# Kernel optimization log

Measured on AMD Instinct MI355X. Metric: run time of the kernel, lower is better.

Reference implementation:

```python
import jax, jax.numpy as jnp
import numpy as np

B, N, K, M, CIN, O, OUT = 4, 1024, 30, 8, 9, 64, 512
BN_SCALE = 1.0 / np.sqrt(1.0 + 1e-5)  # eval-mode BatchNorm with default stats/affine


def setup_inputs() -> dict:
    key = jax.random.key(0)
    ks = jax.random.split(key, 8)
    x = jax.random.normal(ks[0], (B, CIN, N), jnp.float32)
    norm_plt = jax.random.normal(ks[1], (B, 3, N), jnp.float32)
    cls_label = jnp.zeros((B, 16), jnp.float32)
    conv1_w = jax.random.normal(ks[2], (64, 18), jnp.float32) * np.sqrt(2.0 / 18.0)
    conv1_b = jnp.zeros((64,), jnp.float32)
    sn_hw = jax.random.normal(ks[3], (4, 16, 28), jnp.float32) * np.sqrt(2.0 / 28.0)
    sn_ow = jax.random.normal(ks[4], (4, M, 16), jnp.float32) * np.sqrt(2.0 / 16.0)
    sn_ob = jnp.zeros((4, M), jnp.float32)
    mats = jax.random.normal(ks[5], (4, 2 * O, M * O), jnp.float32) * np.sqrt(2.0 / (2.0 * O))
    convt_w = jax.random.normal(ks[6], (OUT, 5 * O), jnp.float32) * np.sqrt(2.0 / (5.0 * O))
    return dict(x=x, norm_plt=norm_plt, cls_label=cls_label, conv1_w=conv1_w,
                conv1_b=conv1_b, sn_hw=sn_hw, sn_ow=sn_ow, sn_ob=sn_ob,
                mats=mats, convt_w=convt_w)


def _gather(feat, idx):
    # feat (B,N,C), idx (B,N,K) int -> (B,N,K,C): neighbor feature gather
    return jax.vmap(lambda f, i: f[i])(feat, idx)


def _bn(t):
    return t * BN_SCALE


def reference(x, norm_plt, cls_label, conv1_w, conv1_b, sn_hw, sn_ow, sn_ob, mats, convt_w):
    xt = jnp.transpose(x, (0, 2, 1))                       # (B,N,9)
    sq = jnp.sum(xt * xt, axis=-1)
    neg_d = 2.0 * jnp.einsum('bic,bjc->bij', xt, xt) - sq[:, :, None] - sq[:, None, :]
    _, idx = jax.lax.top_k(neg_d, K)                       # (B,N,K) knn indices

    nbr = _gather(xt, idx)                                 # (B,N,K,9)
    ctr = jnp.broadcast_to(xt[:, :, None, :], nbr.shape)   # (B,N,K,9)
    diff = nbr - ctr
    ed = jnp.linalg.norm(diff, axis=-1, keepdims=True)     # (B,N,K,1)
    xyz = jnp.concatenate([diff, nbr, ctr, ed], axis=-1)   # (B,N,K,28) scorenet input

    # get_graph_feature -> conv1 (1x1) -> BN -> relu -> max over k
    gf = jnp.concatenate([diff, ctr], axis=-1)             # (B,N,K,18)
    h = jax.nn.relu(_bn(jnp.einsum('bnkc,oc->bnko', gf, conv1_w) + conv1_b))
    x1 = jnp.max(h, axis=2)                                # (B,N,64)

    feats = [x1]
    f = x1
    for l in range(4):  # PAConv layers 2..5 (sequential, fixed count)
        hid = jax.nn.relu(_bn(jnp.einsum('bnkc,hc->bnkh', xyz, sn_hw[l])))
        score = jax.nn.softmax(jnp.einsum('bnkh,mh->bnkm', hid, sn_ow[l]) + sn_ob[l], axis=-1)
        kern = mats[l]                                     # (128, M*64)
        # feat_trans_dgcnn: neighbor uses full kernel on [f;f], center uses top half
        point = (jnp.concatenate([f, f], axis=-1) @ kern).reshape(B, N, M, O)
        center = (f @ kern[:O]).reshape(B, N, M, O)
        # assemble_dgcnn: sum_k sum_m score * (point[knn] - center)
        gp = _gather(point.reshape(B, N, M * O), idx).reshape(B, N, K, M, O)
        out = jnp.einsum('bnkm,bnkmo->bno', score, gp) - jnp.einsum('bnkm,bnmo->bno', score, center)
        f = jax.nn.relu(_bn(out))
        feats.append(f)

    xx = jnp.concatenate(feats, axis=-1)                   # (B,N,320)
    xc = jax.nn.relu(_bn(jnp.einsum('bnc,oc->bno', xx, convt_w)))
    return jnp.max(xc, axis=1)                             # (B,512) global max pool
```

## Files before the change

### kernel.cpp

```cpp
#include <hip/hip_runtime.h>
#include <hip/hip_bf16.h>

#define B 4
#define N 1024
#define KNN 30
#define MM 8
#define HID 16
#define FD 320
#define OUTC 512
#define BNS 0.9999950000374997f

typedef float f32x4 __attribute__((ext_vector_type(4)));
typedef short s16x8 __attribute__((ext_vector_type(8)));

#define OFF_XT16 0
#define OFF_XTT  65536
#define OFF_SQ   102400
#define OFF_IDX  106496
#define OFF_CVT  229376
#define OFF_K2T  311296
#define OFF_FB   442368
#define OFF_SC   1097728

__global__ void __launch_bounds__(256) k_prep(const float* __restrict__ x,
                                              const float* __restrict__ convt_w,
                                              const float* __restrict__ mats,
                                              float* __restrict__ xt16,
                                              float* __restrict__ xtT,
                                              float* __restrict__ sq,
                                              __hip_bfloat16* __restrict__ cvt_bf,
                                              __hip_bfloat16* __restrict__ k2t_bf,
                                              float* __restrict__ out) {
  __shared__ float tile[64][65];
  if (blockIdx.x < 640) {
    int id = blockIdx.x * 256 + threadIdx.x;
    if (id < B * N) {
      int b = id >> 10, n = id & 1023;
      float s = 0.f;
#pragma unroll
      for (int c = 0; c < 9; c++) {
        float v = x[(b * 9 + c) * N + n];
        xt16[id * 16 + c] = v;
        xtT[c * 4096 + id] = v;
        s = fmaf(v, v, s);
      }
      sq[id] = s;
    }
    if (id < B * OUTC) out[id] = 0.f;
    if (id < 512 * 320) cvt_bf[id] = __float2bfloat16(convt_w[id]);
  } else {
    int blk = blockIdx.x - 640;
    int l = blk >> 4, part = (blk >> 3) & 1, m = blk & 7;
    int tr = threadIdx.x >> 6, tc = threadIdx.x & 63;
    const float* src = mats + l * 65536 + (part * 64) * 512 + m * 64;
#pragma unroll
    for (int it = 0; it < 16; it++) { int c = it * 4 + tr; tile[c][tc] = src[c * 512 + tc]; }
    __syncthreads();
    __hip_bfloat16* dst = k2t_bf + l * 65536 + part * 512 + m * 64;
#pragma unroll
    for (int it = 0; it < 16; it++) { int o = it * 4 + tr; dst[o * 1024 + tc] = __float2bfloat16(tile[tc][o]); }
  }
}

__global__ void __launch_bounds__(256) k_knnc1(const float* __restrict__ xt16,
                                               const float* __restrict__ xtT,
                                               const float* __restrict__ sq,
                                               const float* __restrict__ w,
                                               const float* __restrict__ bias,
                                               int* __restrict__ idx,
                                               __hip_bfloat16* __restrict__ feats_bf) {
  int t = threadIdx.x;
  int r = t >> 6;
  int lane = t & 63;
  int row = blockIdx.x * 4 + r;
  int b = row >> 10;
  __shared__ unsigned int hist[4][256];
  __shared__ unsigned int bp[4];
  __shared__ int bn[4];
  __shared__ int js_l[4][KNN];
  __shared__ float ws[64 * 18];
  __shared__ __align__(16) float diff_s[4][KNN][12];
  __shared__ float ctr_s[4][9];
  for (int i = t; i < 64 * 18; i += 256) ws[i] = w[i];
  if (t < 36) { int rr = t / 9, c = t - rr * 9; ctr_s[rr][c] = xt16[(blockIdx.x * 4 + rr) * 16 + c]; }
  const float* xtb = xtT + (b << 10);
  float cx[9];
#pragma unroll
  for (int c = 0; c < 9; c++) cx[c] = xt16[row * 16 + c];
  float sqn = sq[row];
  unsigned int key[16];
#pragma unroll
  for (int s = 0; s < 16; s++) {
    int j = s * 64 + lane;
    float dot = 0.f;
#pragma unroll
    for (int c = 0; c < 9; c++) dot = fmaf(cx[c], xtb[c * 4096 + j], dot);
    float v = 2.0f * dot - sqn - sq[(b << 10) + j];
    unsigned u = __float_as_uint(v);
    key[s] = u ^ ((unsigned)(((int)u) >> 31) | 0x80000000u);
  }
  unsigned prefix = 0; int need = KNN;
  for (int p = 0; p < 4; p++) {
    int shift = 24 - 8 * p;
    for (int i = lane; i < 256; i += 64) hist[r][i] = 0;
    __syncthreads();
    unsigned himask = p ? (0xFFFFFFFFu << (shift + 8)) : 0u;
#pragma unroll
    for (int s = 0; s < 16; s++)
      if ((key[s] & himask) == prefix) atomicAdd(&hist[r][(key[s] >> shift) & 255], 1u);
    __syncthreads();
    int c0 = hist[r][4 * lane], c1 = hist[r][4 * lane + 1];
    int c2 = hist[r][4 * lane + 2], c3 = hist[r][4 * lane + 3];
    int lsum = c0 + c1 + c2 + c3, sfx = lsum;
#pragma unroll
    for (int ofs = 1; ofs < 64; ofs <<= 1) {
      int tt = __shfl_down(sfx, ofs, 64);
      if (lane + ofs < 64) sfx += tt;
    }
    int A3 = sfx - lsum, A2 = A3 + c3, A1 = A2 + c2, A0 = A1 + c1;
    if (A0 < need && need <= A0 + c0) { bp[r] = prefix | ((unsigned)(4 * lane + 0) << shift); bn[r] = need - A0; }
    if (A1 < need && need <= A1 + c1) { bp[r] = prefix | ((unsigned)(4 * lane + 1) << shift); bn[r] = need - A1; }
    if (A2 < need && need <= A2 + c2) { bp[r] = prefix | ((unsigned)(4 * lane + 2) << shift); bn[r] = need - A2; }
    if (A3 < need && need <= A3 + c3) { bp[r] = prefix | ((unsigned)(4 * lane + 3) << shift); bn[r] = need - A3; }
    __syncthreads();
    prefix = bp[r]; need = bn[r];
  }
  unsigned T = prefix;
  int* orow = idx + row * KNN;
  unsigned long long lowmask = (1ull << lane) - 1ull;
  int aboveBase = 0;
#pragma unroll
  for (int s = 0; s < 16; s++) {
    unsigned long long mA = __ballot(key[s] > T);
    if (key[s] > T) {
      int slot = aboveBase + __popcll(mA & lowmask);
      orow[slot] = s * 64 + lane;
      js_l[r][slot] = s * 64 + lane;
    }
    aboveBase += __popcll(mA);
  }
  int tieBase = 0;
  for (int s = 0; s < 16 && tieBase < need; s++) {
    unsigned long long mT = __ballot(key[s] == T);
    if (key[s] == T) {
      int rk = tieBase + __popcll(mT & lowmask);
      if (rk < need) {
        orow[aboveBase + rk] = s * 64 + lane;
        js_l[r][aboveBase + rk] = s * 64 + lane;
      }
    }
    tieBase += __popcll(mT);
  }
  __syncthreads();
  if (t < 120) {
    int rr = t / KNN, k = t - rr * KNN;
    int jg = (b << 10) + js_l[rr][k];
#pragma unroll
    for (int c = 0; c < 9; c++) diff_s[rr][k][c] = xt16[jg * 16 + c] - ctr_s[rr][c];
  }
  __syncthreads();
  float wd[9];
#pragma unroll
  for (int c = 0; c < 9; c++) wd[c] = ws[lane * 18 + c];
  float cd = 0.f;
#pragma unroll
  for (int c = 0; c < 9; c++) cd = fmaf(ctr_s[r][c], ws[lane * 18 + 9 + c], cd);
  float best = -3.0e38f;
  for (int k = 0; k < KNN; k++) {
    const f32x4* dr = (const f32x4*)diff_s[r][k];
    f32x4 d0 = dr[0], d1 = dr[1], d2 = dr[2];
    float dd = 0.f;
    dd = fmaf(d0.x, wd[0], dd); dd = fmaf(d0.y, wd[1], dd);
    dd = fmaf(d0.z, wd[2], dd); dd = fmaf(d0.w, wd[3], dd);
    dd = fmaf(d1.x, wd[4], dd); dd = fmaf(d1.y, wd[5], dd);
    dd = fmaf(d1.z, wd[6], dd); dd = fmaf(d1.w, wd[7], dd);
    dd = fmaf(d2.x, wd[8], dd);
    best = fmaxf(best, dd);
  }
  float val = (best + cd + bias[lane]) * BNS;
  feats_bf[row * FD + lane] = __float2bfloat16(fmaxf(val, 0.f));
}

__global__ void __launch_bounds__(256) k_score(const float* __restrict__ xt16,
                                               const int* __restrict__ idx,
                                               const float* __restrict__ hw,
                                               const float* __restrict__ ow,
                                               const float* __restrict__ ob,
                                               float* __restrict__ score) {
  __shared__ float hws[4 * 448];
  __shared__ float ows[4 * 128];
  __shared__ float obs[32];
  int t = threadIdx.x;
  for (int i = t; i < 1792; i += 256) hws[i] = hw[i];
  for (int i = t; i < 512; i += 256) ows[i] = ow[i];
  if (t < 32) obs[t] = ob[t];
  __syncthreads();
  int id = blockIdx.x * 256 + t;
  int row = id / KNN;
  int b = row >> 10;
  int jg = (b << 10) + idx[id];
  const float* xc = xt16 + row * 16;
  const float* xj = xt16 + jg * 16;
  float xv[28];
  float d2 = 0.f;
#pragma unroll
  for (int c = 0; c < 9; c++) {
    float nb = xj[c], ct = xc[c], df = nb - ct;
    xv[c] = df; xv[9 + c] = nb; xv[18 + c] = ct;
    d2 = fmaf(df, df, d2);
  }
  xv[27] = sqrtf(d2);
  for (int l = 0; l < 4; l++) {
    float hid[HID];
#pragma unroll
    for (int h = 0; h < HID; h++) {
      float a = 0.f;
#pragma unroll
      for (int c = 0; c < 28; c++) a = fmaf(xv[c], hws[l * 448 + h * 28 + c], a);
      hid[h] = fmaxf(a * BNS, 0.f);
    }
    float lg[MM], mx = -3.0e38f;
#pragma unroll
    for (int m = 0; m < MM; m++) {
      float a = obs[l * 8 + m];
#pragma unroll
      for (int h = 0; h < HID; h++) a = fmaf(hid[h], ows[l * 128 + m * 16 + h], a);
      lg[m] = a; mx = fmaxf(mx, a);
    }
    float s = 0.f;
#pragma unroll
    for (int m = 0; m < MM; m++) { lg[m] = __expf(lg[m] - mx); s += lg[m]; }
    float inv = 1.0f / s;
    float* so = score + l * 983040 + id * 8;
    *(float4*)so = make_float4(lg[0] * inv, lg[1] * inv, lg[2] * inv, lg[3] * inv);
    *(float4*)(so + 4) = make_float4(lg[4] * inv, lg[5] * inv, lg[6] * inv, lg[7] * inv);
  }
}

#define HSTR 1048
__global__ void __launch_bounds__(512) k_layer2(const int* __restrict__ idx,
                                                const float* __restrict__ score,
                                                const __hip_bfloat16* __restrict__ k2t_bf,
                                                __hip_bfloat16* __restrict__ feats_bf,
                                                const __hip_bfloat16* __restrict__ cvt_bf,
                                                float* __restrict__ out,
                                                int l, int last) {
  int row0 = blockIdx.x * 16;
  int t = threadIdx.x;
  int b = row0 >> 10;
  __shared__ int js[16][KNN];
  __shared__ float ssum[16][8];
  __shared__ __align__(16) __hip_bfloat16 Hs[16][HSTR];
  __shared__ __align__(16) __hip_bfloat16 ftile[16][336];
  __shared__ float pacc[8][16][16];
  const float* sc_l = score + l * 983040;
  for (int i = t; i < 16 * KNN; i += 512) {
    int r = i / KNN, k = i - r * KNN;
    js[r][k] = (b << 10) + idx[(row0 + r) * KNN + k];
  }
  if (t < 128) {
    int r = t >> 3, m = t & 7;
    float a = 0.f;
    for (int k = 0; k < KNN; k++) a += sc_l[(row0 + r) * 240 + k * 8 + m];
    ssum[r][m] = a;
  }
  __syncthreads();
  int w = t >> 6, lane = t & 63;
#pragma unroll
  for (int rr = 0; rr < 2; rr++) {
    int r = w * 2 + rr;
    int row = row0 + r;
    const float4* srow = (const float4*)(sc_l + row * 240);
    float g[MM] = {};
#pragma unroll
    for (int k = 0; k < KNN; k++) {
      float fv = __bfloat162float(feats_bf[js[r][k] * FD + l * 64 + lane]);
      float4 s0 = srow[2 * k], s1 = srow[2 * k + 1];
      g[0] = fmaf(s0.x, fv, g[0]); g[1] = fmaf(s0.y, fv, g[1]);
      g[2] = fmaf(s0.z, fv, g[2]); g[3] = fmaf(s0.w, fv, g[3]);
      g[4] = fmaf(s1.x, fv, g[4]); g[5] = fmaf(s1.y, fv, g[5]);
      g[6] = fmaf(s1.z, fv, g[6]); g[7] = fmaf(s1.w, fv, g[7]);
    }
    float fn = __bfloat162float(feats_bf[row * FD + l * 64 + lane]);
#pragma unroll
    for (int m = 0; m < MM; m++) {
      Hs[r][m * 64 + lane] = __float2bfloat16(g[m] - ssum[r][m] * fn);
      Hs[r][512 + m * 64 + lane] = __float2bfloat16(g[m]);
    }
  }
  if (last) {
    const short* Fs = (const short*)feats_bf;
    for (int i = t; i < 512; i += 512) {}
    for (int i = t; i < 512; i += 512) {}
    for (int i = t; i < 512; i += 512) {}
  }
  __syncthreads();
  if (last) {
    const short* Fs = (const short*)feats_bf;
    for (int i = t; i < 512; i += 512) {
      int r = i >> 5, c8 = (i & 31) * 8;
      *(s16x8*)&ftile[r][c8] = *(const s16x8*)(Fs + (row0 + r) * FD + c8);
    }
    __syncthreads();
  }
  int lr = lane & 15, lk8 = (lane >> 4) * 8;
  {
    int ct = w & 3, kh = w >> 2;
    const short* Ks2 = (const short*)(k2t_bf + l * 65536);
    const short* brow = Ks2 + (ct * 16 + lr) * 1024 + kh * 512 + lk8;
    const short* arow = (const short*)&Hs[lr][kh * 512 + lk8];
    f32x4 acc = {0.f, 0.f, 0.f, 0.f};
#pragma unroll 8
    for (int kk = 0; kk < 16; kk++) {
      s16x8 a = *(const s16x8*)(arow + kk * 32);
      s16x8 bb = *(const s16x8*)(brow + kk * 32);
      acc = __builtin_amdgcn_mfma_f32_16x16x32_bf16(a, bb, acc, 0, 0, 0);
    }
#pragma unroll
    for (int i = 0; i < 4; i++)
      pacc[w][(lane >> 4) * 4 + i][lr] = acc[i];
  }
  __syncthreads();
  if (w < 4) {
#pragma unroll
    for (int i = 0; i < 4; i++) {
      int ri = (lane >> 4) * 4 + i;
      float val = fmaxf((pacc[w][ri][lr] + pacc[w + 4][ri][lr]) * BNS, 0.f);
      __hip_bfloat16 vb = __float2bfloat16(val);
      if (!last) {
        feats_bf[(row0 + ri) * FD + (l + 1) * 64 + w * 16 + lr] = vb;
      } else {
        ftile[ri][256 + w * 16 + lr] = vb;
      }
    }
  }
  if (last) {
    __syncthreads();
    const short* Ws = (const short*)cvt_bf;
#pragma unroll
    for (int tn = 0; tn < 4; tn++) {
      int nb = w * 64 + tn * 16;
      const short* brow = Ws + (nb + lr) * FD + lk8;
      const short* arow = (const short*)&ftile[lr][lk8];
      f32x4 acc = {0.f, 0.f, 0.f, 0.f};
#pragma unroll
      for (int kk = 0; kk < 10; kk++) {
        s16x8 a = *(const s16x8*)(arow + kk * 32);
        s16x8 bb = *(const s16x8*)(brow + kk * 32);
        acc = __builtin_amdgcn_mfma_f32_16x16x32_bf16(a, bb, acc, 0, 0, 0);
      }
      float mx = fmaxf(fmaxf(acc[0], acc[1]), fmaxf(acc[2], acc[3]));
      mx = fmaxf(mx, __shfl_xor(mx, 16, 64));
      mx = fmaxf(mx, __shfl_xor(mx, 32, 64));
      if ((lane >> 4) == 0) {
        float val = fmaxf(mx * BNS, 0.f);
        atomicMax((unsigned int*)out + b * OUTC + nb + lr, __float_as_uint(val));
      }
    }
  }
}

extern "C" void kernel_launch(void* const* d_in, const int* in_sizes, int n_in,
                              void* d_out, int out_size, void* d_ws, size_t ws_size,
                              hipStream_t stream) {
  const float* x       = (const float*)d_in[0];
  const float* conv1_w = (const float*)d_in[3];
  const float* conv1_b = (const float*)d_in[4];
  const float* sn_hw   = (const float*)d_in[5];
  const float* sn_ow   = (const float*)d_in[6];
  const float* sn_ob   = (const float*)d_in[7];
  const float* mats    = (const float*)d_in[8];
  const float* convt_w = (const float*)d_in[9];
  float* out = (float*)d_out;

  float* wsp = (float*)d_ws;
  float* xt16 = wsp + OFF_XT16;
  float* xtT  = wsp + OFF_XTT;
  float* sq   = wsp + OFF_SQ;
  int* idx    = (int*)(wsp + OFF_IDX);
  __hip_bfloat16* cvt_bf = (__hip_bfloat16*)(wsp + OFF_CVT);
  __hip_bfloat16* k2t_bf = (__hip_bfloat16*)(wsp + OFF_K2T);
  __hip_bfloat16* feats_bf = (__hip_bfloat16*)(wsp + OFF_FB);
  float* score = wsp + OFF_SC;

  k_prep<<<704, 256, 0, stream>>>(x, convt_w, mats, xt16, xtT, sq, cvt_bf, k2t_bf, out);
  k_knnc1<<<1024, 256, 0, stream>>>(xt16, xtT, sq, conv1_w, conv1_b, idx, feats_bf);
  k_score<<<480, 256, 0, stream>>>(xt16, idx, sn_hw, sn_ow, sn_ob, score);
  for (int l = 0; l < 4; l++) {
    k_layer2<<<256, 512, 0, stream>>>(idx, score, k2t_bf, feats_bf, cvt_bf, out,
                                      l, l == 3 ? 1 : 0);
  }
}
```

Measured before the change: 192.9 us.

## Fuse kNN, conv1 and ScoreNet into one kernel; precompute score sums

Removes the transposed x buffers: the kNN kernel now reads x directly and computes squared norms inline. ScoreNet softmax is folded into the same kernel, reusing the neighbor and diff values already staged in shared memory. The per-row score sums are computed there and passed to the layer kernels through a global buffer. This drops one launch and the intermediate traffic, but only 120 of 256 threads do the ScoreNet work, which may lengthen that kernel's critical path.

```diff
diff --git a/kernel.cpp b/kernel.cpp
--- a/kernel.cpp
+++ b/kernel.cpp
@@ -13,89 +13,94 @@
 typedef float f32x4 __attribute__((ext_vector_type(4)));
 typedef short s16x8 __attribute__((ext_vector_type(8)));
 
-#define OFF_XT16 0
-#define OFF_XTT  65536
-#define OFF_SQ   102400
-#define OFF_IDX  106496
-#define OFF_CVT  229376
-#define OFF_K2T  311296
-#define OFF_FB   442368
-#define OFF_SC   1097728
-
-__global__ void __launch_bounds__(256) k_prep(const float* __restrict__ x,
-                                              const float* __restrict__ convt_w,
-                                              const float* __restrict__ mats,
-                                              float* __restrict__ xt16,
-                                              float* __restrict__ xtT,
-                                              float* __restrict__ sq,
-                                              __hip_bfloat16* __restrict__ cvt_bf,
-                                              __hip_bfloat16* __restrict__ k2t_bf,
-                                              float* __restrict__ out) {
+#define OFF_IDX  0
+#define OFF_CVT  122880
+#define OFF_K2T  204800
+#define OFF_FB   335872
+#define OFF_SC   991232
+#define OFF_SSUM 4923392
+
+__global__ void __launch_bounds__(256) k_prep2(const float* __restrict__ mats,
+                                               const float* __restrict__ convt_w,
+                                               __hip_bfloat16* __restrict__ k2t_bf,
+                                               __hip_bfloat16* __restrict__ cvt_bf,
+                                               float* __restrict__ out) {
   __shared__ float tile[64][65];
-  if (blockIdx.x < 640) {
-    int id = blockIdx.x * 256 + threadIdx.x;
-    if (id < B * N) {
-      int b = id >> 10, n = id & 1023;
-      float s = 0.f;
-#pragma unroll
-      for (int c = 0; c < 9; c++) {
-        float v = x[(b * 9 + c) * N + n];
-        xt16[id * 16 + c] = v;
-        xtT[c * 4096 + id] = v;
-        s = fmaf(v, v, s);
-      }
-      sq[id] = s;
+  int t = threadIdx.x;
+  if (blockIdx.x < 64) {
+    int blk = blockIdx.x;
+    int l = blk >> 4, part = (blk >> 3) & 1, m = blk & 7;
+    int tr = t >> 6, tc = t & 63;
+    const float* src = mats + l * 65536 + (part * 64) * 512 + m * 64;
+#pragma unroll
+    for (int it = 0; it < 16; it++) { int c = it * 4 + tr; tile[c][tc] = src[c * 512 + tc]; }
+    __syncthreads();
+    __hip_bfloat16* dst = k2t_bf + l * 65536 + part * 512 + m * 64;
+#pragma unroll
+    for (int it = 0; it < 16; it++) { int o = it * 4 + tr; dst[o * 1024 + tc] = __float2bfloat16(tile[tc][o]); }
+  } else {
+    int id = (blockIdx.x - 64) * 256 + t;
+#pragma unroll
+    for (int q = 0; q < 4; q++) {
+      int i = id + q * 40960;
+      cvt_bf[i] = __float2bfloat16(convt_w[i]);
     }
     if (id < B * OUTC) out[id] = 0.f;
-    if (id < 512 * 320) cvt_bf[id] = __float2bfloat16(convt_w[id]);
-  } else {
-    int blk = blockIdx.x - 640;
-    int l = blk >> 4, part = (blk >> 3) & 1, m = blk & 7;
-    int tr = threadIdx.x >> 6, tc = threadIdx.x & 63;
-    const float* src = mats + l * 65536 + (part * 64) * 512 + m * 64;
-#pragma unroll
-    for (int it = 0; it < 16; it++) { int c = it * 4 + tr; tile[c][tc] = src[c * 512 + tc]; }
-    __syncthreads();
-    __hip_bfloat16* dst = k2t_bf + l * 65536 + part * 512 + m * 64;
-#pragma unroll
-    for (int it = 0; it < 16; it++) { int o = it * 4 + tr; dst[o * 1024 + tc] = __float2bfloat16(tile[tc][o]); }
   }
 }
 
-__global__ void __launch_bounds__(256) k_knnc1(const float* __restrict__ xt16,
-                                               const float* __restrict__ xtT,
-                                               const float* __restrict__ sq,
-                                               const float* __restrict__ w,
-                                               const float* __restrict__ bias,
-                                               int* __restrict__ idx,
-                                               __hip_bfloat16* __restrict__ feats_bf) {
+__global__ void __launch_bounds__(256) k1(const float* __restrict__ x,
+                                          const float* __restrict__ conv1_w,
+                                          const float* __restrict__ conv1_b,
+                                          const float* __restrict__ hw,
+                                          const float* __restrict__ ow,
+                                          const float* __restrict__ ob,
+                                          int* __restrict__ idx,
+                                          __hip_bfloat16* __restrict__ feats_bf,
+                                          float* __restrict__ score,
+                                          float* __restrict__ ssum_g) {
   int t = threadIdx.x;
-  int r = t >> 6;
-  int lane = t & 63;
+  int r = t >> 6, lane = t & 63;
   int row = blockIdx.x * 4 + r;
   int b = row >> 10;
   __shared__ unsigned int hist[4][256];
   __shared__ unsigned int bp[4];
   __shared__ int bn[4];
   __shared__ int js_l[4][KNN];
-  __shared__ float ws[64 * 18];
+  __shared__ float ws[1152];
+  __shared__ float hws[1792], ows[512], obs[32];
   __shared__ __align__(16) float diff_s[4][KNN][12];
+  __shared__ __align__(16) float nbr_s[4][KNN][12];
   __shared__ float ctr_s[4][9];
-  for (int i = t; i < 64 * 18; i += 256) ws[i] = w[i];
-  if (t < 36) { int rr = t / 9, c = t - rr * 9; ctr_s[rr][c] = xt16[(blockIdx.x * 4 + rr) * 16 + c]; }
-  const float* xtb = xtT + (b << 10);
+  __shared__ float scl[4][KNN][8];
+  const float* xb = x + b * 9216;
+
+  for (int i = t; i < 1152; i += 256) ws[i] = conv1_w[i];
+  for (int i = t; i < 1792; i += 256) hws[i] = hw[i];
+  if (t < 512) { }
+  for (int i = t; i < 512; i += 256) ows[i] = ow[i];
+  if (t < 32) obs[t] = ob[t];
+  if (t < 36) { int rr = t / 9, c = t - rr * 9; ctr_s[rr][c] = xb[c * 1024 + ((blockIdx.x * 4 + rr) & 1023)]; }
+
+  int jrow = row & 1023;
   float cx[9];
 #pragma unroll
-  for (int c = 0; c < 9; c++) cx[c] = xt16[row * 16 + c];
-  float sqn = sq[row];
+  for (int c = 0; c < 9; c++) cx[c] = xb[c * 1024 + jrow];
+  float sqn = 0.f;
+#pragma unroll
+  for (int c = 0; c < 9; c++) sqn = fmaf(cx[c], cx[c], sqn);
   unsigned int key[16];
 #pragma unroll
   for (int s = 0; s < 16; s++) {
     int j = s * 64 + lane;
-    float dot = 0.f;
-#pragma unroll
-    for (int c = 0; c < 9; c++) dot = fmaf(cx[c], xtb[c * 4096 + j], dot);
-    float v = 2.0f * dot - sqn - sq[(b << 10) + j];
+    float dot = 0.f, sbj = 0.f;
+#pragma unroll
+    for (int c = 0; c < 9; c++) {
+      float xjc = xb[c * 1024 + j];
+      dot = fmaf(cx[c], xjc, dot);
+      sbj = fmaf(xjc, xjc, sbj);
+    }
+    float v = 2.0f * dot - sqn - sbj;
     unsigned u = __float_as_uint(v);
     key[s] = u ^ ((unsigned)(((int)u) >> 31) | 0x80000000u);
   }
@@ -152,94 +157,102 @@
     tieBase += __popcll(mT);
   }
   __syncthreads();
+
   if (t < 120) {
     int rr = t / KNN, k = t - rr * KNN;
-    int jg = (b << 10) + js_l[rr][k];
-#pragma unroll
-    for (int c = 0; c < 9; c++) diff_s[rr][k][c] = xt16[jg * 16 + c] - ctr_s[rr][c];
-  }
-  __syncthreads();
-  float wd[9];
-#pragma unroll
-  for (int c = 0; c < 9; c++) wd[c] = ws[lane * 18 + c];
-  float cd = 0.f;
-#pragma unroll
-  for (int c = 0; c < 9; c++) cd = fmaf(ctr_s[r][c], ws[lane * 18 + 9 + c], cd);
-  float best = -3.0e38f;
-  for (int k = 0; k < KNN; k++) {
-    const f32x4* dr = (const f32x4*)diff_s[r][k];
-    f32x4 d0 = dr[0], d1 = dr[1], d2 = dr[2];
-    float dd = 0.f;
-    dd = fmaf(d0.x, wd[0], dd); dd = fmaf(d0.y, wd[1], dd);
-    dd = fmaf(d0.z, wd[2], dd); dd = fmaf(d0.w, wd[3], dd);
-    dd = fmaf(d1.x, wd[4], dd); dd = fmaf(d1.y, wd[5], dd);
-    dd = fmaf(d1.z, wd[6], dd); dd = fmaf(d1.w, wd[7], dd);
-    dd = fmaf(d2.x, wd[8], dd);
-    best = fmaxf(best, dd);
-  }
-  float val = (best + cd + bias[lane]) * BNS;
-  feats_bf[row * FD + lane] = __float2bfloat16(fmaxf(val, 0.f));
-}
-
-__global__ void __launch_bounds__(256) k_score(const float* __restrict__ xt16,
-                                               const int* __restrict__ idx,
-                                               const float* __restrict__ hw,
-                                               const float* __restrict__ ow,
-                                               const float* __restrict__ ob,
-                                               float* __restrict__ score) {
-  __shared__ float hws[4 * 448];
-  __shared__ float ows[4 * 128];
-  __shared__ float obs[32];
-  int t = threadIdx.x;
-  for (int i = t; i < 1792; i += 256) hws[i] = hw[i];
-  for (int i = t; i < 512; i += 256) ows[i] = ow[i];
-  if (t < 32) obs[t] = ob[t];
-  __syncthreads();
-  int id = blockIdx.x * 256 + t;
-  int row = id / KNN;
-  int b = row >> 10;
-  int jg = (b << 10) + idx[id];
-  const float* xc = xt16 + row * 16;
-  const float* xj = xt16 + jg * 16;
+    int j = js_l[rr][k];
+#pragma unroll
+    for (int c = 0; c < 9; c++) {
+      float nb = xb[c * 1024 + j];
+      nbr_s[rr][k][c] = nb;
+      diff_s[rr][k][c] = nb - ctr_s[rr][c];
+    }
+  }
+  __syncthreads();
+
+  {
+    float wd[9];
+#pragma unroll
+    for (int c = 0; c < 9; c++) wd[c] = ws[lane * 18 + c];
+    float cd = 0.f;
+#pragma unroll
+    for (int c = 0; c < 9; c++) cd = fmaf(ctr_s[r][c], ws[lane * 18 + 9 + c], cd);
+    float best = -3.0e38f;
+    for (int k = 0; k < KNN; k++) {
+      const f32x4* dr = (const f32x4*)diff_s[r][k];
+      f32x4 d0 = dr[0], d1 = dr[1], d2 = dr[2];
+      float dd = 0.f;
+      dd = fmaf(d0.x, wd[0], dd); dd = fmaf(d0.y, wd[1], dd);
+      dd = fmaf(d0.z, wd[2], dd); dd = fmaf(d0.w, wd[3], dd);
+      dd = fmaf(d1.x, wd[4], dd); dd = fmaf(d1.y, wd[5], dd);
+      dd = fmaf(d1.z, wd[6], dd); dd = fmaf(d1.w, wd[7], dd);
+      dd = fmaf(d2.x, wd[8], dd);
+      best = fmaxf(best, dd);
+    }
+    float val = (best + cd + conv1_b[lane]) * BNS;
+    feats_bf[row * FD + lane] = __float2bfloat16(fmaxf(val, 0.f));
+  }
+
   float xv[28];
-  float d2 = 0.f;
-#pragma unroll
-  for (int c = 0; c < 9; c++) {
-    float nb = xj[c], ct = xc[c], df = nb - ct;
-    xv[c] = df; xv[9 + c] = nb; xv[18 + c] = ct;
-    d2 = fmaf(df, df, d2);
-  }
-  xv[27] = sqrtf(d2);
+  int rrS = 0, kS = 0;
+  if (t < 120) {
+    rrS = t / KNN; kS = t - rrS * KNN;
+    float d2 = 0.f;
+#pragma unroll
+    for (int c = 0; c < 9; c++) {
+      float df = diff_s[rrS][kS][c];
+      xv[c] = df; xv[9 + c] = nbr_s[rrS][kS][c]; xv[18 + c] = ctr_s[rrS][c];
+      d2 = fmaf(df, df, d2);
+    }
+    xv[27] = sqrtf(d2);
+  }
   for (int l = 0; l < 4; l++) {
-    float hid[HID];
-#pragma unroll
-    for (int h = 0; h < HID; h++) {
+    if (t < 120) {
+      float hid[HID];
+#pragma unroll
+      for (int h = 0; h < HID; h++) {
+        float a = 0.f;
+#pragma unroll
+        for (int c = 0; c < 28; c++) a = fmaf(xv[c], hws[l * 448 + h * 28 + c], a);
+        hid[h] = fmaxf(a * BNS, 0.f);
+      }
+      float lg[MM], mx = -3.0e38f;
+#pragma unroll
+      for (int m = 0; m < MM; m++) {
+        float a = obs[l * 8 + m];
+#pragma unroll
+        for (int h = 0; h < HID; h++) a = fmaf(hid[h], ows[l * 128 + m * 16 + h], a);
+        lg[m] = a; mx = fmaxf(mx, a);
+      }
+      float s = 0.f;
+#pragma unroll
+      for (int m = 0; m < MM; m++) { lg[m] = __expf(lg[m] - mx); s += lg[m]; }
+      float inv = 1.0f / s;
+      int rowr = blockIdx.x * 4 + rrS;
+      float* so = score + l * 983040 + (rowr * KNN + kS) * 8;
+      float sv0 = lg[0] * inv, sv1 = lg[1] * inv, sv2 = lg[2] * inv, sv3 = lg[3] * inv;
+      float sv4 = lg[4] * inv, sv5 = lg[5] * inv, sv6 = lg[6] * inv, sv7 = lg[7] * inv;
+      *(float4*)so = make_float4(sv0, sv1, sv2, sv3);
+      *(float4*)(so + 4) = make_float4(sv4, sv5, sv6, sv7);
+      scl[rrS][kS][0] = sv0; scl[rrS][kS][1] = sv1; scl[rrS][kS][2] = sv2; scl[rrS][kS][3] = sv3;
+      scl[rrS][kS][4] = sv4; scl[rrS][kS][5] = sv5; scl[rrS][kS][6] = sv6; scl[rrS][kS][7] = sv7;
+    }
+    __syncthreads();
+    if (t < 32) {
+      int rr = t >> 3, m = t & 7;
       float a = 0.f;
 #pragma unroll
-      for (int c = 0; c < 28; c++) a = fmaf(xv[c], hws[l * 448 + h * 28 + c], a);
-      hid[h] = fmaxf(a * BNS, 0.f);
-    }
-    float lg[MM], mx = -3.0e38f;
-#pragma unroll
-    for (int m = 0; m < MM; m++) {
-      float a = obs[l * 8 + m];
-#pragma unroll
-      for (int h = 0; h < HID; h++) a = fmaf(hid[h], ows[l * 128 + m * 16 + h], a);
-      lg[m] = a; mx = fmaxf(mx, a);
-    }
-    float s = 0.f;
-#pragma unroll
-    for (int m = 0; m < MM; m++) { lg[m] = __expf(lg[m] - mx); s += lg[m]; }
-    float inv = 1.0f / s;
-    float* so = score + l * 983040 + id * 8;
-    *(float4*)so = make_float4(lg[0] * inv, lg[1] * inv, lg[2] * inv, lg[3] * inv);
-    *(float4*)(so + 4) = make_float4(lg[4] * inv, lg[5] * inv, lg[6] * inv, lg[7] * inv);
+      for (int k = 0; k < KNN; k++) a += scl[rr][k][m];
+      ssum_g[l * 32768 + (blockIdx.x * 4 + rr) * 8 + m] = a;
+    }
+    __syncthreads();
   }
 }
 
 #define HSTR 1048
 __global__ void __launch_bounds__(512) k_layer2(const int* __restrict__ idx,
                                                 const float* __restrict__ score,
+                                                const float* __restrict__ ssum_g,
                                                 const __hip_bfloat16* __restrict__ k2t_bf,
                                                 __hip_bfloat16* __restrict__ feats_bf,
                                                 const __hip_bfloat16* __restrict__ cvt_bf,
@@ -258,12 +271,7 @@
     int r = i / KNN, k = i - r * KNN;
     js[r][k] = (b << 10) + idx[(row0 + r) * KNN + k];
   }
-  if (t < 128) {
-    int r = t >> 3, m = t & 7;
-    float a = 0.f;
-    for (int k = 0; k < KNN; k++) a += sc_l[(row0 + r) * 240 + k * 8 + m];
-    ssum[r][m] = a;
-  }
+  if (t < 128) ssum[t >> 3][t & 7] = ssum_g[l * 32768 + (row0 + (t >> 3)) * 8 + (t & 7)];
   __syncthreads();
   int w = t >> 6, lane = t & 63;
 #pragma unroll
@@ -288,17 +296,11 @@
       Hs[r][512 + m * 64 + lane] = __float2bfloat16(g[m]);
     }
   }
+  __syncthreads();
   if (last) {
     const short* Fs = (const short*)feats_bf;
-    for (int i = t; i < 512; i += 512) {}
-    for (int i = t; i < 512; i += 512) {}
-    for (int i = t; i < 512; i += 512) {}
-  }
-  __syncthreads();
-  if (last) {
-    const short* Fs = (const short*)feats_bf;
-    for (int i = t; i < 512; i += 512) {
-      int r = i >> 5, c8 = (i & 31) * 8;
+    {
+      int r = t >> 5, c8 = (t & 31) * 8;
       *(s16x8*)&ftile[r][c8] = *(const s16x8*)(Fs + (row0 + r) * FD + c8);
     }
     __syncthreads();
@@ -374,20 +376,18 @@
   float* out = (float*)d_out;
 
   float* wsp = (float*)d_ws;
-  float* xt16 = wsp + OFF_XT16;
-  float* xtT  = wsp + OFF_XTT;
-  float* sq   = wsp + OFF_SQ;
   int* idx    = (int*)(wsp + OFF_IDX);
   __hip_bfloat16* cvt_bf = (__hip_bfloat16*)(wsp + OFF_CVT);
   __hip_bfloat16* k2t_bf = (__hip_bfloat16*)(wsp + OFF_K2T);
   __hip_bfloat16* feats_bf = (__hip_bfloat16*)(wsp + OFF_FB);
   float* score = wsp + OFF_SC;
-
-  k_prep<<<704, 256, 0, stream>>>(x, convt_w, mats, xt16, xtT, sq, cvt_bf, k2t_bf, out);
-  k_knnc1<<<1024, 256, 0, stream>>>(xt16, xtT, sq, conv1_w, conv1_b, idx, feats_bf);
-  k_score<<<480, 256, 0, stream>>>(xt16, idx, sn_hw, sn_ow, sn_ob, score);
+  float* ssum_g = wsp + OFF_SSUM;
+
+  k_prep2<<<224, 256, 0, stream>>>(mats, convt_w, k2t_bf, cvt_bf, out);
+  k1<<<1024, 256, 0, stream>>>(x, conv1_w, conv1_b, sn_hw, sn_ow, sn_ob,
+                               idx, feats_bf, score, ssum_g);
   for (int l = 0; l < 4; l++) {
-    k_layer2<<<256, 512, 0, stream>>>(idx, score, k2t_bf, feats_bf, cvt_bf, out,
-                                      l, l == 3 ? 1 : 0);
+    k_layer2<<<256, 512, 0, stream>>>(idx, score, ssum_g, k2t_bf, feats_bf,
+                                      cvt_bf, out, l, l == 3 ? 1 : 0);
   }
 }
```

Result: faster. 187.0 us (-3.1%).
